# Optimization experiments

Hardware: AMD Instinct MI355X
Metric: run time of the kernel (lower is better)

The kernel has to match this reference:

```python
import jax, jax.numpy as jnp
import numpy as np

N_NODES = 100_000
N_EDGES = 800_000
NODE_DIM = 192
CONF_DIM = 64
HID = 256  # graphsage_in == graphsage_hidden
ALPHA = 0.2  # LeakyReLU negative slope


def _lrelu(x):
    return jnp.where(x >= 0, x, ALPHA * x)


def _sage_max(x, src, dst, wl, bl, wr):
    # PyG SAGEConv, aggr='max': out = lin_l(max_{j in N(i)} x_j) + lin_r(x_i)
    msgs = x[src]                                   # [E, HID] gather
    agg = jax.ops.segment_max(msgs, dst, num_segments=N_NODES)  # [N, HID]
    agg = jnp.where(jnp.isneginf(agg), 0.0, agg)    # isolated nodes -> 0
    return agg @ wl + bl + x @ wr


def _mlp2(x, w0, b0, w1, b1):
    # Linear -> LeakyReLU(0.2) -> Linear (activation only between layers)
    return _lrelu(x @ w0 + b0) @ w1 + b1


def setup_inputs() -> dict:
    key = jax.random.key(0)
    ks = jax.random.split(key, 16)
    s = 0.05
    inp = {
        "node_features": jax.random.normal(ks[0], (N_NODES, NODE_DIM), jnp.float32),
        "config_features": jax.random.normal(ks[1], (N_NODES, CONF_DIM), jnp.float32),
        "edges": jax.random.randint(ks[2], (2, N_EDGES), 0, N_NODES, jnp.int32),
        "prenet_w0": jax.random.normal(ks[3], (HID, NODE_DIM), jnp.float32) * s,
        "prenet_b0": jnp.zeros((NODE_DIM,), jnp.float32),
        "prenet_w1": jax.random.normal(ks[4], (NODE_DIM, NODE_DIM), jnp.float32) * s,
        "prenet_b1": jnp.zeros((NODE_DIM,), jnp.float32),
    }
    for l, k0 in ((0, 5), (1, 10)):
        inp[f"sage{l}_wl"] = jax.random.normal(ks[k0], (HID, HID), jnp.float32) * s
        inp[f"sage{l}_bl"] = jnp.zeros((HID,), jnp.float32)
        inp[f"sage{l}_wr"] = jax.random.normal(ks[k0 + 1], (HID, HID), jnp.float32) * s
        inp[f"mlp{l}_w0"] = jax.random.normal(ks[k0 + 2], (HID, NODE_DIM), jnp.float32) * s
        inp[f"mlp{l}_b0"] = jnp.zeros((NODE_DIM,), jnp.float32)
        inp[f"mlp{l}_w1"] = jax.random.normal(ks[k0 + 3], (NODE_DIM, NODE_DIM), jnp.float32) * s
        inp[f"mlp{l}_b1"] = jnp.zeros((NODE_DIM,), jnp.float32)
    return inp


def reference(node_features, config_features, edges,
              prenet_w0, prenet_b0, prenet_w1, prenet_b1,
              sage0_wl, sage0_bl, sage0_wr, mlp0_w0, mlp0_b0, mlp0_w1, mlp0_b1,
              sage1_wl, sage1_bl, sage1_wr, mlp1_w0, mlp1_b0, mlp1_w1, mlp1_b1):
    src, dst = edges[0], edges[1]
    x = jnp.concatenate([config_features, node_features], axis=1)  # [N, 256]
    x = _lrelu(_mlp2(x, prenet_w0, prenet_b0, prenet_w1, prenet_b1))  # [N, 192]
    layers = [
        (sage0_wl, sage0_bl, sage0_wr, mlp0_w0, mlp0_b0, mlp0_w1, mlp0_b1),
        (sage1_wl, sage1_bl, sage1_wr, mlp1_w0, mlp1_b0, mlp1_w1, mlp1_b1),
    ]
    for swl, sbl, swr, mw0, mb0, mw1, mb1 in layers:
        y = jnp.concatenate([config_features, x], axis=1)          # [N, 256]
        y = _sage_max(y, src, dst, swl, sbl, swr)                  # [N, 256]
        y = _lrelu(_mlp2(y, mw0, mb0, mw1, mb1))                   # [N, 192]
        x = x + y
    return x
```

## Files before the change

kernel.cpp:

```cpp
#include <hip/hip_runtime.h>
#include <stdint.h>

#define N_NODES 100000
#define N_EDGES 800000

typedef unsigned short u16;
typedef __attribute__((ext_vector_type(8))) short bf16x8;
typedef __attribute__((ext_vector_type(8))) unsigned short ushort8;
typedef __attribute__((ext_vector_type(4))) float f32x4;
typedef __attribute__((ext_vector_type(4))) int i32x4;
typedef __attribute__((ext_vector_type(4))) unsigned int u32x4;

struct alignas(8) U16x4 { u16 x, y, z, w; };

__device__ __forceinline__ u16 f2b(float f) {
    union { float f; unsigned u; } x; x.f = f;
    unsigned r = (x.u + 0x7FFFu + ((x.u >> 16) & 1u)) >> 16;
    return (u16)r;
}
__device__ __forceinline__ float b2f(u16 h) {
    union { unsigned u; float f; } x; x.u = ((unsigned)h) << 16;
    return x.f;
}
__device__ __forceinline__ u16 keyb(u16 h) {
    u16 m = (u16)((short)h >> 15);
    return (u16)(h ^ (0x8000u | (m & 0x7FFFu)));
}
__device__ __forceinline__ u16 unkey(u16 k) {
    u16 m = (u16)((short)k >> 15);
    return (u16)(k ^ (0x8000u | (~m & 0x7FFFu)));
}
__device__ __forceinline__ unsigned pkmax(unsigned a, unsigned b) {
    unsigned d;
    asm("v_pk_max_u16 %0, %1, %2" : "=v"(d) : "v"(a), "v"(b));
    return d;
}
__device__ __forceinline__ u32x4 pkmax4(u32x4 a, u32x4 b) {
    u32x4 r;
    r.x = pkmax(a.x, b.x); r.y = pkmax(a.y, b.y);
    r.z = pkmax(a.z, b.z); r.w = pkmax(a.w, b.w);
    return r;
}

__device__ __forceinline__ void gload_lds16(const void* g, void* l) {
    __builtin_amdgcn_global_load_lds(
        (const __attribute__((address_space(1))) char*)(uintptr_t)g,
        (__attribute__((address_space(3))) char*)(uintptr_t)l,
        16, 0, 0);
}

__device__ __forceinline__ int simgG(int row, int col) { return row * 136 + col; }
__device__ __forceinline__ int simgF(int row, int col) { return row * 200 + col; }


__global__ void k_prep(const float* __restrict__ conf, const float* __restrict__ node,
                       u16* __restrict__ conf16, u16* __restrict__ node16,
                       u16* __restrict__ keyed, int* __restrict__ deg) {
    const int c4 = N_NODES * 64 / 4;
    const int n4 = N_NODES * 192 / 4;
    int i = blockIdx.x * blockDim.x + threadIdx.x;
    if (i < c4) {
        float4 v = ((const float4*)conf)[i];
        U16x4 o; o.x = f2b(v.x); o.y = f2b(v.y); o.z = f2b(v.z); o.w = f2b(v.w);
        ((U16x4*)conf16)[i] = o;
        U16x4 ko; ko.x = keyb(o.x); ko.y = keyb(o.y); ko.z = keyb(o.z); ko.w = keyb(o.w);
        int n = i >> 4;
        ((U16x4*)keyed)[n * 64 + (i & 15)] = ko;
    } else if (i < c4 + n4) {
        float4 v = ((const float4*)node)[i - c4];
        U16x4 o; o.x = f2b(v.x); o.y = f2b(v.y); o.z = f2b(v.z); o.w = f2b(v.w);
        ((U16x4*)node16)[i - c4] = o;
    } else if (i < c4 + n4 + N_NODES / 4) {
        i32x4 z = {0, 0, 0, 0};
        ((i32x4*)deg)[i - c4 - n4] = z;
    }
}


struct PackSeg { const float* a; const float* b; u16* dst; int K0, K1, Ncol, beg, end; };
struct PackArgs { PackSeg s[8]; };

__global__ void k_pack(PackArgs p, int total) {
    int idx = blockIdx.x * blockDim.x + threadIdx.x;
    if (idx >= total) return;
    #pragma unroll
    for (int si = 0; si < 8; ++si) {
        if (idx >= p.s[si].beg && idx < p.s[si].end) {
            int li = idx - p.s[si].beg;
            int Ncol = p.s[si].Ncol, K0 = p.s[si].K0;
            int kq = li & 7;
            int t = li >> 3;
            int c15 = t & 15; t >>= 4;
            int k8 = t & 3;  t >>= 2;
            int nb = Ncol >> 4;
            int cb = t % nb;
            int ks = t / nb;
            int col = cb * 16 + c15;
            int k = ks * 32 + k8 * 8 + kq;
            float v = (k < K0) ? p.s[si].a[(size_t)k * Ncol + col]
                               : p.s[si].b[(size_t)(k - K0) * Ncol + col];
            p.s[si].dst[li] = f2b(v);
        }
    }
}


__global__ void k_count(const int* __restrict__ dst, int* __restrict__ deg) {
    int e = blockIdx.x * blockDim.x + threadIdx.x;
    if (e < N_EDGES) atomicAdd(&deg[dst[e]], 1);
}

__global__ void k_scan1(const int* __restrict__ deg, int* __restrict__ excl,
                        int* __restrict__ bsum, int n) {
    __shared__ int sh[512];
    int t = threadIdx.x;
    int base = blockIdx.x * 2048 + t * 4;
    int v0 = (base + 0 < n) ? deg[base + 0] : 0;
    int v1 = (base + 1 < n) ? deg[base + 1] : 0;
    int v2 = (base + 2 < n) ? deg[base + 2] : 0;
    int v3 = (base + 3 < n) ? deg[base + 3] : 0;
    int tot = v0 + v1 + v2 + v3;
    sh[t] = tot;
    __syncthreads();
    for (int off = 1; off < 512; off <<= 1) {
        int x = (t >= off) ? sh[t - off] : 0;
        __syncthreads();
        sh[t] += x;
        __syncthreads();
    }
    int run = sh[t] - tot;
    if (base + 0 < n) excl[base + 0] = run; run += v0;
    if (base + 1 < n) excl[base + 1] = run; run += v1;
    if (base + 2 < n) excl[base + 2] = run; run += v2;
    if (base + 3 < n) excl[base + 3] = run;
    if (t == 511) bsum[blockIdx.x] = sh[t];
}

__global__ void k_scan2(int* __restrict__ bsum, int nb) {
    __shared__ int sh[64];
    int t = threadIdx.x;
    int v = (t < nb) ? bsum[t] : 0;
    sh[t] = v;
    __syncthreads();
    for (int off = 1; off < 64; off <<= 1) {
        int x = (t >= off) ? sh[t - off] : 0;
        __syncthreads();
        sh[t] += x;
        __syncthreads();
    }
    if (t < nb) bsum[t] = sh[t] - v;
}

__global__ void k_scan3(int* __restrict__ excl, const int* __restrict__ bsum,
                        int* __restrict__ cursor, int n) {
    int i = blockIdx.x * blockDim.x + threadIdx.x;
    if (i < n) {
        int v = excl[i] + bsum[i >> 11];
        excl[i] = v;
        cursor[i] = v;
    }
}

__global__ void k_scatter(const int* __restrict__ src, const int* __restrict__ dst,
                          int* __restrict__ cursor, int* __restrict__ esrc) {
    int e = blockIdx.x * blockDim.x + threadIdx.x;
    if (e < N_EDGES) {
        int p = atomicAdd(&cursor[dst[e]], 1);
        esrc[p] = src[e];
    }
}


template<int CHUNKS>
__global__ __launch_bounds__(256) void k_agg(
    const u16* __restrict__ keyed,
    const int* __restrict__ indptr, const int* __restrict__ deg,
    const int* __restrict__ iend, const int* __restrict__ esrc,
    u16* __restrict__ agg, u16* __restrict__ aggC) {
    __shared__ int se[512];
    __shared__ int sinfo[2];
    const int b4 = blockIdx.x * 4;
    if (threadIdx.x == 0) {
        sinfo[0] = indptr[b4];
        sinfo[1] = iend[b4 + 3];
    }
    __syncthreads();
    const int sbase = sinfo[0];
    const int slen = sinfo[1] - sbase;
    const bool useLds = slen <= 512;
    if (useLds) {
        for (int i = threadIdx.x; i < slen; i += 256) se[i] = esrc[sbase + i];
    }
    __syncthreads();

    const int node = b4 + (threadIdx.x >> 6);
    const int lane = threadIdx.x & 63;
    constexpr int ACTIVE = (CHUNKS == 32) ? 64 : 48;
    const int e_sub = (CHUNKS == 32) ? (lane >> 5) : (lane >= 24 ? 1 : 0);
    int ch = lane - e_sub * CHUNKS;
    if (ch < 0 || ch >= CHUNKS) ch = 0;
    const int start = indptr[node];
    const int d = deg[node];
    const u16* bp = keyed + ((CHUNKS == 32) ? 0 : 64) + ch * 8;

    u32x4 m = {0u, 0u, 0u, 0u};

    if (lane < ACTIVE && d > 0) {
        const int rounds = (d + 15) >> 4;
        const int lbase = start - sbase;
        const int dm1 = d - 1;
        for (int rr = 0; rr < rounds; ++rr) {
            const int b0 = rr * 16 + e_sub;
            int s[8];
            if (useLds) {
                #pragma unroll
                for (int t = 0; t < 8; ++t) s[t] = se[lbase + min(b0 + 2 * t, dm1)];
            } else {
                #pragma unroll
                for (int t = 0; t < 8; ++t) s[t] = esrc[start + min(b0 + 2 * t, dm1)];
            }
            u32x4 v0 = *(const u32x4*)(bp + (size_t)s[0] * 256);
            u32x4 v1 = *(const u32x4*)(bp + (size_t)s[1] * 256);
            u32x4 v2 = *(const u32x4*)(bp + (size_t)s[2] * 256);
            u32x4 v3 = *(const u32x4*)(bp + (size_t)s[3] * 256);
            u32x4 v4 = *(const u32x4*)(bp + (size_t)s[4] * 256);
            u32x4 v5 = *(const u32x4*)(bp + (size_t)s[5] * 256);
            u32x4 v6 = *(const u32x4*)(bp + (size_t)s[6] * 256);
            u32x4 v7 = *(const u32x4*)(bp + (size_t)s[7] * 256);
            u32x4 a = pkmax4(pkmax4(v0, v1), pkmax4(v2, v3));
            u32x4 b = pkmax4(pkmax4(v4, v5), pkmax4(v6, v7));
            m = pkmax4(m, pkmax4(a, b));
        }
    }

    if (CHUNKS == 32) {
        m.x = pkmax(m.x, __shfl_xor(m.x, 32, 64));
        m.y = pkmax(m.y, __shfl_xor(m.y, 32, 64));
        m.z = pkmax(m.z, __shfl_xor(m.z, 32, 64));
        m.w = pkmax(m.w, __shfl_xor(m.w, 32, 64));
    } else {
        m.x = pkmax(m.x, __shfl(m.x, lane + 24, 64));
        m.y = pkmax(m.y, __shfl(m.y, lane + 24, 64));
        m.z = pkmax(m.z, __shfl(m.z, lane + 24, 64));
        m.w = pkmax(m.w, __shfl(m.w, lane + 24, 64));
    }

    unsigned wv[4] = {m.x, m.y, m.z, m.w};
    ushort8 o;
    #pragma unroll
    for (int j = 0; j < 4; ++j) {
        u16 klo = (u16)(wv[j] & 0xFFFFu), khi = (u16)(wv[j] >> 16);
        o[2 * j]     = (d > 0) ? unkey(klo) : (u16)0;
        o[2 * j + 1] = (d > 0) ? unkey(khi) : (u16)0;
    }

    if (CHUNKS == 32) {
        if (lane < 32) {
            *(ushort8*)(agg + (size_t)node * 256 + lane * 8) = o;
            if (lane < 8)
                *(ushort8*)(aggC + (size_t)node * 64 + lane * 8) = o;
        }
    } else {
        if (lane < 24) {
            *(ushort8*)(agg + (size_t)node * 256 + 64 + lane * 8) = o;
        } else if (lane >= 48 && lane < 56) {
            const int c2 = lane - 48;
            ushort8 v = *(const ushort8*)(aggC + (size_t)node * 64 + c2 * 8);
            *(ushort8*)(agg + (size_t)node * 256 + c2 * 8) = v;
        }
    }
}


template<int BN>
__global__ __launch_bounds__(512) void k_gemm(
    const u16* __restrict__ A0, int K0,
    const u16* __restrict__ A1, int K1,
    const u16* __restrict__ A2, int K2,
    const u16* __restrict__ Bt,
    const float* __restrict__ bias,
    u16* __restrict__ outb,
    int nrows)
{
    constexpr int FN = BN / 64;
    constexpr int ASZ = 128 * 32;
    __shared__ u16 lds[2][ASZ + BN * 32] __attribute__((aligned(16)));

    const int tid = threadIdx.x;
    const int wave = tid >> 6;
    const int lane = tid & 63;
    const int wr = wave >> 2;
    const int wc = wave & 3;
    const int rowbase = blockIdx.x * 128;
    const int nk = (K0 + K1 + K2) >> 5;

    const int arow = ((tid >> 6) << 4) | (tid & 15);
    int grow = rowbase + arow; if (grow >= nrows) grow = nrows - 1;
    const int ak8 = (tid >> 4) & 3;
    const u16* segp[3] = {A0, A1, A2};
    const int segK[3] = {K0, K1, K2};
    int seg = 0;
    const u16* gA = segp[0] + (size_t)grow * segK[0] + ak8 * 8;
    int segleft = segK[0] >> 5;
    const u16* gB0 = Bt + (size_t)tid * 8;
    const u16* gB1 = Bt + (size_t)(512 + tid) * 8;
    const int wb = wave * 512;

    auto adv = [&]() {
        gA += 32;
        if (--segleft == 0) {
            while (seg < 2) {
                ++seg;
                if (segK[seg] > 0) {
                    gA = segp[seg] + (size_t)grow * segK[seg] + ak8 * 8;
                    segleft = segK[seg] >> 5;
                    break;
                }
            }
        }
        gB0 += BN * 32;
        gB1 += BN * 32;
    };
    auto stage = [&](int buf) {
        gload_lds16(gA, &lds[buf][wb]);
        gload_lds16(gB0, &lds[buf][ASZ + wb]);
        if constexpr (BN == 256) {
            gload_lds16(gB1, &lds[buf][ASZ + 4096 + wb]);
        } else {
            if (tid < 256) gload_lds16(gB1, &lds[buf][ASZ + 4096 + wb]);
        }
    };

    f32x4 zero = {0.f, 0.f, 0.f, 0.f};
    f32x4 acc[4][FN];
    #pragma unroll
    for (int fm = 0; fm < 4; ++fm)
        #pragma unroll
        for (int fn = 0; fn < FN; ++fn)
            acc[fm][fn] = zero;

    stage(0); adv();
    __syncthreads();

    const int l15 = lane & 15, l4 = lane >> 4;

    for (int ks = 0; ks < nk; ++ks) {
        const int cur = ks & 1;
        if (ks + 1 < nk) { stage(cur ^ 1); adv(); }
        const u16* la = &lds[cur][0];
        const u16* lb = &lds[cur][ASZ];
        bf16x8 a[4], b[FN];
        #pragma unroll
        for (int fm = 0; fm < 4; ++fm)
            a[fm] = *(const bf16x8*)(la + (wr * 4 + fm) * 512 + lane * 8);
        #pragma unroll
        for (int fn = 0; fn < FN; ++fn)
            b[fn] = *(const bf16x8*)(lb + (wc * FN + fn) * 512 + lane * 8);
        #pragma unroll
        for (int fm = 0; fm < 4; ++fm)
            #pragma unroll
            for (int fn = 0; fn < FN; ++fn)
                acc[fm][fn] = __builtin_amdgcn_mfma_f32_16x16x32_bf16(a[fm], b[fn], acc[fm][fn], 0, 0, 0);
        __syncthreads();
    }

    u16* sbuf = &lds[0][0];
    #pragma unroll
    for (int chunk = 0; chunk < 2; ++chunk) {
        if ((wc >> 1) == chunk) {
            const int cbase = (wc & 1) * 64;
            #pragma unroll
            for (int fn = 0; fn < FN; ++fn) {
                const int cp = cbase + fn * 16 + l15;
                const float bs = bias[chunk * 128 + cp];
                #pragma unroll
                for (int fm = 0; fm < 4; ++fm) {
                    const int rbase = wr * 64 + fm * 16 + l4 * 4;
                    #pragma unroll
                    for (int r = 0; r < 4; ++r)
                        sbuf[simgG(rbase + r, cp)] = f2b(acc[fm][fn][r] + bs);
                }
            }
        }
        __syncthreads();
        #pragma unroll
        for (int j = 0; j < 4; ++j) {
            const int chk = j * 512 + tid;
            const int row = chk >> 4;
            const int cp = (chk & 15) * 8;
            const int gr = rowbase + row;
            if (gr < nrows) {
                ushort8 hv = *(const ushort8*)&sbuf[simgG(row, cp)];
                *(ushort8*)(outb + (size_t)gr * 256 + chunk * 128 + cp) = hv;
            }
        }
        __syncthreads();
    }
}


template<int EPI>
__global__ __launch_bounds__(512) void k_fused(
    const u16* __restrict__ A0, int K0,
    const u16* __restrict__ A1, int K1,
    const u16* __restrict__ B1t, const float* __restrict__ bias1,
    const u16* __restrict__ B2t, const float* __restrict__ bias2,
    float* __restrict__ outf, u16* __restrict__ outb,
    const u16* __restrict__ resid16, u16* __restrict__ keyed,
    int nrows)
{
    __shared__ u16 lds[25592] __attribute__((aligned(16)));

    const int tid = threadIdx.x;
    const int wave = tid >> 6;
    const int lane = tid & 63;
    const int wr = wave >> 2;
    const int wc = wave & 3;
    const int l15 = lane & 15, l4 = lane >> 4;
    const int rowbase = blockIdx.x * 128;
    const int nk1 = (K0 + K1) >> 5;

    const int arow = ((tid >> 6) << 4) | (tid & 15);
    int grow = rowbase + arow; if (grow >= nrows) grow = nrows - 1;
    const int ak8 = (tid >> 4) & 3;
    const u16* gA = A0 + (size_t)grow * K0 + ak8 * 8;
    int segleft = K0 >> 5;
    const u16* gB0 = B1t + (size_t)tid * 8;
    const u16* gB1 = B1t + (size_t)(512 + tid) * 8;
    const int wb = wave * 512;

    auto adv = [&]() {
        gA += 32;
        if (--segleft == 0 && K1 > 0) {
            gA = A1 + (size_t)grow * K1 + ak8 * 8;
            segleft = K1 >> 5;
        }
        gB0 += 6144;
        gB1 += 6144;
    };
    auto stage = [&](int buf) {
        gload_lds16(gA, &lds[buf * 4096 + wb]);
        gload_lds16(gB0, &lds[8192 + buf * 6144 + wb]);
        if (tid < 256) gload_lds16(gB1, &lds[8192 + buf * 6144 + 4096 + wb]);
    };

    f32x4 zero = {0.f, 0.f, 0.f, 0.f};
    f32x4 acc[4][3];
    #pragma unroll
    for (int fm = 0; fm < 4; ++fm)
        #pragma unroll
        for (int fn = 0; fn < 3; ++fn)
            acc[fm][fn] = zero;

    stage(0); adv();
    __syncthreads();

    for (int ks = 0; ks < nk1; ++ks) {
        const int cur = ks & 1;
        if (ks + 1 < nk1) { stage(cur ^ 1); adv(); }
        const u16* la = &lds[cur * 4096];
        const u16* lb = &lds[8192 + cur * 6144];
        bf16x8 a[4], b[3];
        #pragma unroll
        for (int fm = 0; fm < 4; ++fm)
            a[fm] = *(const bf16x8*)(la + (wr * 4 + fm) * 512 + lane * 8);
        #pragma unroll
        for (int fn = 0; fn < 3; ++fn)
            b[fn] = *(const bf16x8*)(lb + (wc * 3 + fn) * 512 + lane * 8);
        #pragma unroll
        for (int fm = 0; fm < 4; ++fm)
            #pragma unroll
            for (int fn = 0; fn < 3; ++fn)
                acc[fm][fn] = __builtin_amdgcn_mfma_f32_16x16x32_bf16(a[fm], b[fn], acc[fm][fn], 0, 0, 0);
        __syncthreads();
    }

    {
        const int c0 = wc * 48;
        #pragma unroll
        for (int fn = 0; fn < 3; ++fn) {
            const int c = c0 + fn * 16 + l15;
            const float bs = bias1[c];
            const int coff = (c >> 5) * 4096 + ((c >> 3) & 3) * 128 + (c & 7);
            #pragma unroll
            for (int fm = 0; fm < 4; ++fm) {
                const int rb = wr * 4 + fm;
                #pragma unroll
                for (int rr = 0; rr < 4; ++rr) {
                    const int r16 = l4 * 4 + rr;
                    float v = acc[fm][fn][rr] + bs;
                    v = (v >= 0.f) ? v : 0.2f * v;
                    lds[coff + rb * 512 + r16 * 8] = f2b(v);
                }
            }
        }
    }
    __syncthreads();

    bf16x8 breg[18];
    #pragma unroll
    for (int ks = 0; ks < 6; ++ks)
        #pragma unroll
        for (int fn = 0; fn < 3; ++fn)
            breg[ks * 3 + fn] = *(const bf16x8*)(B2t + (size_t)(ks * 12 + wc * 3 + fn) * 512 + lane * 8);

    f32x4 acc2[4][3];
    #pragma unroll
    for (int fm = 0; fm < 4; ++fm)
        #pragma unroll
        for (int fn = 0; fn < 3; ++fn)
            acc2[fm][fn] = zero;

    #pragma unroll
    for (int ks = 0; ks < 6; ++ks) {
        bf16x8 a2[4];
        #pragma unroll
        for (int fm = 0; fm < 4; ++fm)
            a2[fm] = *(const bf16x8*)(&lds[ks * 4096 + (wr * 4 + fm) * 512 + lane * 8]);
        #pragma unroll
        for (int fm = 0; fm < 4; ++fm)
            #pragma unroll
            for (int fn = 0; fn < 3; ++fn)
                acc2[fm][fn] = __builtin_amdgcn_mfma_f32_16x16x32_bf16(a2[fm], breg[ks * 3 + fn], acc2[fm][fn], 0, 0, 0);
    }
    __syncthreads();

    {
        const int c0 = wc * 48;
        #pragma unroll
        for (int fn = 0; fn < 3; ++fn) {
            const int c = c0 + fn * 16 + l15;
            const float bs = bias2[c];
            #pragma unroll
            for (int fm = 0; fm < 4; ++fm) {
                const int rbase = wr * 64 + fm * 16 + l4 * 4;
                #pragma unroll
                for (int r = 0; r < 4; ++r) {
                    float v = acc2[fm][fn][r] + bs;
                    v = (v >= 0.f) ? v : 0.2f * v;
                    lds[simgF(rbase + r, c)] = f2b(v);
                }
            }
        }
    }
    __syncthreads();

    #pragma unroll
    for (int j = 0; j < 6; ++j) {
        const int chk = j * 512 + tid;
        const int row = chk / 24;
        const int c = (chk - row * 24) * 8;
        const int gr = rowbase + row;
        if (gr < nrows) {
            ushort8 hv = *(const ushort8*)&lds[simgF(row, c)];
            if (EPI == 4) {
                ushort8 rv = *(const ushort8*)(resid16 + (size_t)gr * 192 + c);
                f32x4 o0, o1;
                #pragma unroll
                for (int k = 0; k < 4; ++k) {
                    o0[k] = b2f(hv[k]) + b2f(rv[k]);
                    o1[k] = b2f(hv[k + 4]) + b2f(rv[k + 4]);
                }
                *(f32x4*)(outf + (size_t)gr * 192 + c) = o0;
                *(f32x4*)(outf + (size_t)gr * 192 + c + 4) = o1;
            } else if (EPI == 5) {
                *(ushort8*)(outb + (size_t)gr * 192 + c) = hv;
                ushort8 kv;
                #pragma unroll
                for (int k = 0; k < 8; ++k) kv[k] = keyb(hv[k]);
                *(ushort8*)(keyed + (size_t)gr * 256 + 64 + c) = kv;
            } else {
                ushort8 rv = *(const ushort8*)(resid16 + (size_t)gr * 192 + c);
                ushort8 nb, kv;
                #pragma unroll
                for (int k = 0; k < 8; ++k) {
                    u16 hb = f2b(b2f(hv[k]) + b2f(rv[k]));
                    nb[k] = hb;
                    kv[k] = keyb(hb);
                }
                *(ushort8*)(outb + (size_t)gr * 192 + c) = nb;
                *(ushort8*)(keyed + (size_t)gr * 256 + 64 + c) = kv;
            }
        }
    }
}


extern "C" void kernel_launch(void* const* d_in, const int* in_sizes, int n_in,
                              void* d_out, int out_size, void* d_ws, size_t ws_size,
                              hipStream_t stream)
{
    (void)in_sizes; (void)n_in; (void)out_size; (void)ws_size;
    const float* node = (const float*)d_in[0];
    const float* conf = (const float*)d_in[1];
    const int* edges  = (const int*)d_in[2];
    const float* pw0  = (const float*)d_in[3];
    const float* pb0  = (const float*)d_in[4];
    const float* pw1  = (const float*)d_in[5];
    const float* pb1  = (const float*)d_in[6];
    const float* W[14];
    for (int i = 0; i < 14; ++i) W[i] = (const float*)d_in[7 + i];
    float* out = (float*)d_out;
    const int* e_src = edges;
    const int* e_dst = edges + N_EDGES;

    u16* keyed = (u16*)d_out;

    char* w = (char*)d_ws;
    auto alloc = [&](size_t b) { char* p = w; w += (b + 255) & ~(size_t)255; return p; };
    u16* conf16 = (u16*)alloc((size_t)N_NODES * 64 * 2);
    u16* node16 = (u16*)alloc((size_t)N_NODES * 192 * 2);
    u16* x16    = (u16*)alloc((size_t)N_NODES * 192 * 2);
    u16* agg16  = (u16*)alloc((size_t)N_NODES * 256 * 2);
    u16* aggC   = (u16*)alloc((size_t)N_NODES * 64 * 2);
    int* deg    = (int*)alloc((size_t)N_NODES * 4);
    int* indptr = (int*)alloc((size_t)N_NODES * 4);
    int* cursor = (int*)alloc((size_t)N_NODES * 4);
    int* esrc   = (int*)alloc((size_t)N_EDGES * 4);
    int* bsum   = (int*)alloc(4096);
    u16* pw0t   = (u16*)alloc((size_t)192 * 256 * 2);
    u16* pw1t   = (u16*)alloc((size_t)192 * 192 * 2);
    u16 *sB[2], *mw0t[2], *mw1t[2];
    for (int l = 0; l < 2; ++l) {
        sB[l]   = (u16*)alloc((size_t)256 * 512 * 2);
        mw0t[l] = (u16*)alloc((size_t)192 * 256 * 2);
        mw1t[l] = (u16*)alloc((size_t)192 * 192 * 2);
    }

    {
        const int tot = N_NODES * 64 / 4 + N_NODES * 192 / 4 + N_NODES / 4;
        k_prep<<<(tot + 255) / 256, 256, 0, stream>>>(conf, node, conf16, node16, keyed, deg);
    }
    {
        PackArgs pa;
        int off = 0;
        auto seg = [&](int i, const float* a, int K0, const float* b, int K1, int Ncol, u16* dst) {
            int sz = Ncol * (K0 + K1);
            pa.s[i] = {a, b, dst, K0, K1, Ncol, off, off + sz};
            off += sz;
        };
        seg(0, pw0, 256, nullptr, 0, 192, pw0t);
        seg(1, pw1, 192, nullptr, 0, 192, pw1t);
        seg(2, W[0], 256, W[2], 256, 256, sB[0]);
        seg(3, W[3], 256, nullptr, 0, 192, mw0t[0]);
        seg(4, W[5], 192, nullptr, 0, 192, mw1t[0]);
        seg(5, W[7], 256, W[9], 256, 256, sB[1]);
        seg(6, W[10], 256, nullptr, 0, 192, mw0t[1]);
        seg(7, W[12], 192, nullptr, 0, 192, mw1t[1]);
        k_pack<<<(off + 255) / 256, 256, 0, stream>>>(pa, off);
    }
    k_count<<<(N_EDGES + 255) / 256, 256, 0, stream>>>(e_dst, deg);
    int nb = (N_NODES + 2047) / 2048;
    k_scan1<<<nb, 512, 0, stream>>>(deg, indptr, bsum, N_NODES);
    k_scan2<<<1, 64, 0, stream>>>(bsum, nb);
    k_scan3<<<(N_NODES + 255) / 256, 256, 0, stream>>>(indptr, bsum, cursor, N_NODES);
    k_scatter<<<(N_EDGES + 255) / 256, 256, 0, stream>>>(e_src, e_dst, cursor, esrc);

    const int gblk = (N_NODES + 127) / 128;
    k_fused<5><<<gblk, 512, 0, stream>>>(conf16, 64, node16, 192,
                                         pw0t, pb0, pw1t, pb1,
                                         nullptr, x16, nullptr, keyed, N_NODES);
    for (int l = 0; l < 2; ++l) {
        if (l == 0)
            k_agg<32><<<N_NODES / 4, 256, 0, stream>>>(keyed, indptr, deg, cursor, esrc, agg16, aggC);
        else
            k_agg<24><<<N_NODES / 4, 256, 0, stream>>>(keyed, indptr, deg, cursor, esrc, agg16, aggC);
        k_gemm<256><<<gblk, 512, 0, stream>>>(agg16, 256, conf16, 64, x16, 192,
                                              sB[l], W[7*l+1], agg16, N_NODES);
        if (l == 0)
            k_fused<6><<<gblk, 512, 0, stream>>>(agg16, 256, nullptr, 0,
                                                 mw0t[0], W[4], mw1t[0], W[6],
                                                 nullptr, x16, x16, keyed, N_NODES);
        else
            k_fused<4><<<gblk, 512, 0, stream>>>(agg16, 256, nullptr, 0,
                                                 mw0t[1], W[11], mw1t[1], W[13],
                                                 out, nullptr, x16, nullptr, N_NODES);
    }
}
```

Before: 444.8 us.

## Merge weight packing into prep, persistent agg grid, read conf agg via strided GEMM segments

Folds the weight-packing kernel into the input-prep kernel to save a launch. Makes the aggregation kernel grid-stride over node quads with a fixed 2048-block grid instead of one block per quad. Generalises the GEMM A-operand to four strided segments so layer 1 reads the config aggregate from aggC directly, which removes the per-node copy of aggC into agg16. The persistent loop adds an extra barrier per quad and may reduce latency hiding in the gather.

```diff
diff --git a/kernel.cpp b/kernel.cpp
--- a/kernel.cpp
+++ b/kernel.cpp
@@ -53,9 +53,14 @@
 __device__ __forceinline__ int simgF(int row, int col) { return row * 200 + col; }
 
 
+struct PackSeg { const float* a; const float* b; u16* dst; int K0, K1, Ncol, beg, end; };
+struct PackArgs { PackSeg s[8]; };
+
+
 __global__ void k_prep(const float* __restrict__ conf, const float* __restrict__ node,
                        u16* __restrict__ conf16, u16* __restrict__ node16,
-                       u16* __restrict__ keyed, int* __restrict__ deg) {
+                       u16* __restrict__ keyed, int* __restrict__ deg,
+                       PackArgs p, int packTotal) {
     const int c4 = N_NODES * 64 / 4;
     const int n4 = N_NODES * 192 / 4;
     int i = blockIdx.x * blockDim.x + threadIdx.x;
@@ -73,33 +78,28 @@
     } else if (i < c4 + n4 + N_NODES / 4) {
         i32x4 z = {0, 0, 0, 0};
         ((i32x4*)deg)[i - c4 - n4] = z;
-    }
-}
-
-
-struct PackSeg { const float* a; const float* b; u16* dst; int K0, K1, Ncol, beg, end; };
-struct PackArgs { PackSeg s[8]; };
-
-__global__ void k_pack(PackArgs p, int total) {
-    int idx = blockIdx.x * blockDim.x + threadIdx.x;
-    if (idx >= total) return;
-    #pragma unroll
-    for (int si = 0; si < 8; ++si) {
-        if (idx >= p.s[si].beg && idx < p.s[si].end) {
-            int li = idx - p.s[si].beg;
-            int Ncol = p.s[si].Ncol, K0 = p.s[si].K0;
-            int kq = li & 7;
-            int t = li >> 3;
-            int c15 = t & 15; t >>= 4;
-            int k8 = t & 3;  t >>= 2;
-            int nb = Ncol >> 4;
-            int cb = t % nb;
-            int ks = t / nb;
-            int col = cb * 16 + c15;
-            int k = ks * 32 + k8 * 8 + kq;
-            float v = (k < K0) ? p.s[si].a[(size_t)k * Ncol + col]
-                               : p.s[si].b[(size_t)(k - K0) * Ncol + col];
-            p.s[si].dst[li] = f2b(v);
+    } else {
+        int idx = i - (c4 + n4 + N_NODES / 4);
+        if (idx < packTotal) {
+            #pragma unroll
+            for (int si = 0; si < 8; ++si) {
+                if (idx >= p.s[si].beg && idx < p.s[si].end) {
+                    int li = idx - p.s[si].beg;
+                    int Ncol = p.s[si].Ncol, K0 = p.s[si].K0;
+                    int kq = li & 7;
+                    int t = li >> 3;
+                    int c15 = t & 15; t >>= 4;
+                    int k8 = t & 3;  t >>= 2;
+                    int nb = Ncol >> 4;
+                    int cb = t % nb;
+                    int ks = t / nb;
+                    int col = cb * 16 + c15;
+                    int k = ks * 32 + k8 * 8 + kq;
+                    float v = (k < K0) ? p.s[si].a[(size_t)k * Ncol + col]
+                                       : p.s[si].b[(size_t)(k - K0) * Ncol + col];
+                    p.s[si].dst[li] = f2b(v);
+                }
+            }
         }
     }
 }
@@ -176,107 +176,106 @@
     const u16* __restrict__ keyed,
     const int* __restrict__ indptr, const int* __restrict__ deg,
     const int* __restrict__ iend, const int* __restrict__ esrc,
-    u16* __restrict__ agg, u16* __restrict__ aggC) {
+    u16* __restrict__ agg, u16* __restrict__ aggC, int nquads) {
     __shared__ int se[512];
     __shared__ int sinfo[2];
-    const int b4 = blockIdx.x * 4;
-    if (threadIdx.x == 0) {
-        sinfo[0] = indptr[b4];
-        sinfo[1] = iend[b4 + 3];
-    }
-    __syncthreads();
-    const int sbase = sinfo[0];
-    const int slen = sinfo[1] - sbase;
-    const bool useLds = slen <= 512;
-    if (useLds) {
-        for (int i = threadIdx.x; i < slen; i += 256) se[i] = esrc[sbase + i];
-    }
-    __syncthreads();
-
-    const int node = b4 + (threadIdx.x >> 6);
     const int lane = threadIdx.x & 63;
     constexpr int ACTIVE = (CHUNKS == 32) ? 64 : 48;
     const int e_sub = (CHUNKS == 32) ? (lane >> 5) : (lane >= 24 ? 1 : 0);
     int ch = lane - e_sub * CHUNKS;
     if (ch < 0 || ch >= CHUNKS) ch = 0;
-    const int start = indptr[node];
-    const int d = deg[node];
     const u16* bp = keyed + ((CHUNKS == 32) ? 0 : 64) + ch * 8;
 
-    u32x4 m = {0u, 0u, 0u, 0u};
-
-    if (lane < ACTIVE && d > 0) {
-        const int rounds = (d + 15) >> 4;
-        const int lbase = start - sbase;
-        const int dm1 = d - 1;
-        for (int rr = 0; rr < rounds; ++rr) {
-            const int b0 = rr * 16 + e_sub;
-            int s[8];
-            if (useLds) {
-                #pragma unroll
-                for (int t = 0; t < 8; ++t) s[t] = se[lbase + min(b0 + 2 * t, dm1)];
-            } else {
-                #pragma unroll
-                for (int t = 0; t < 8; ++t) s[t] = esrc[start + min(b0 + 2 * t, dm1)];
-            }
-            u32x4 v0 = *(const u32x4*)(bp + (size_t)s[0] * 256);
-            u32x4 v1 = *(const u32x4*)(bp + (size_t)s[1] * 256);
-            u32x4 v2 = *(const u32x4*)(bp + (size_t)s[2] * 256);
-            u32x4 v3 = *(const u32x4*)(bp + (size_t)s[3] * 256);
-            u32x4 v4 = *(const u32x4*)(bp + (size_t)s[4] * 256);
-            u32x4 v5 = *(const u32x4*)(bp + (size_t)s[5] * 256);
-            u32x4 v6 = *(const u32x4*)(bp + (size_t)s[6] * 256);
-            u32x4 v7 = *(const u32x4*)(bp + (size_t)s[7] * 256);
-            u32x4 a = pkmax4(pkmax4(v0, v1), pkmax4(v2, v3));
-            u32x4 b = pkmax4(pkmax4(v4, v5), pkmax4(v6, v7));
-            m = pkmax4(m, pkmax4(a, b));
-        }
-    }
-
-    if (CHUNKS == 32) {
-        m.x = pkmax(m.x, __shfl_xor(m.x, 32, 64));
-        m.y = pkmax(m.y, __shfl_xor(m.y, 32, 64));
-        m.z = pkmax(m.z, __shfl_xor(m.z, 32, 64));
-        m.w = pkmax(m.w, __shfl_xor(m.w, 32, 64));
-    } else {
-        m.x = pkmax(m.x, __shfl(m.x, lane + 24, 64));
-        m.y = pkmax(m.y, __shfl(m.y, lane + 24, 64));
-        m.z = pkmax(m.z, __shfl(m.z, lane + 24, 64));
-        m.w = pkmax(m.w, __shfl(m.w, lane + 24, 64));
-    }
-
-    unsigned wv[4] = {m.x, m.y, m.z, m.w};
-    ushort8 o;
-    #pragma unroll
-    for (int j = 0; j < 4; ++j) {
-        u16 klo = (u16)(wv[j] & 0xFFFFu), khi = (u16)(wv[j] >> 16);
-        o[2 * j]     = (d > 0) ? unkey(klo) : (u16)0;
-        o[2 * j + 1] = (d > 0) ? unkey(khi) : (u16)0;
-    }
-
-    if (CHUNKS == 32) {
-        if (lane < 32) {
-            *(ushort8*)(agg + (size_t)node * 256 + lane * 8) = o;
-            if (lane < 8)
-                *(ushort8*)(aggC + (size_t)node * 64 + lane * 8) = o;
-        }
-    } else {
-        if (lane < 24) {
-            *(ushort8*)(agg + (size_t)node * 256 + 64 + lane * 8) = o;
-        } else if (lane >= 48 && lane < 56) {
-            const int c2 = lane - 48;
-            ushort8 v = *(const ushort8*)(aggC + (size_t)node * 64 + c2 * 8);
-            *(ushort8*)(agg + (size_t)node * 256 + c2 * 8) = v;
-        }
-    }
-}
-
+    for (int q = blockIdx.x; q < nquads; q += gridDim.x) {
+        const int b4 = q * 4;
+        if (threadIdx.x == 0) {
+            sinfo[0] = indptr[b4];
+            sinfo[1] = iend[b4 + 3];
+        }
+        __syncthreads();
+        const int sbase = sinfo[0];
+        const int slen = sinfo[1] - sbase;
+        const bool useLds = slen <= 512;
+        if (useLds) {
+            for (int i = threadIdx.x; i < slen; i += 256) se[i] = esrc[sbase + i];
+        }
+        __syncthreads();
+
+        const int node = b4 + (threadIdx.x >> 6);
+        const int start = indptr[node];
+        const int d = deg[node];
+
+        u32x4 m = {0u, 0u, 0u, 0u};
+
+        if (lane < ACTIVE && d > 0) {
+            const int rounds = (d + 15) >> 4;
+            const int lbase = start - sbase;
+            const int dm1 = d - 1;
+            for (int rr = 0; rr < rounds; ++rr) {
+                const int b0 = rr * 16 + e_sub;
+                int s[8];
+                if (useLds) {
+                    #pragma unroll
+                    for (int t = 0; t < 8; ++t) s[t] = se[lbase + min(b0 + 2 * t, dm1)];
+                } else {
+                    #pragma unroll
+                    for (int t = 0; t < 8; ++t) s[t] = esrc[start + min(b0 + 2 * t, dm1)];
+                }
+                u32x4 v0 = *(const u32x4*)(bp + (size_t)s[0] * 256);
+                u32x4 v1 = *(const u32x4*)(bp + (size_t)s[1] * 256);
+                u32x4 v2 = *(const u32x4*)(bp + (size_t)s[2] * 256);
+                u32x4 v3 = *(const u32x4*)(bp + (size_t)s[3] * 256);
+                u32x4 v4 = *(const u32x4*)(bp + (size_t)s[4] * 256);
+                u32x4 v5 = *(const u32x4*)(bp + (size_t)s[5] * 256);
+                u32x4 v6 = *(const u32x4*)(bp + (size_t)s[6] * 256);
+                u32x4 v7 = *(const u32x4*)(bp + (size_t)s[7] * 256);
+                u32x4 a = pkmax4(pkmax4(v0, v1), pkmax4(v2, v3));
+                u32x4 b = pkmax4(pkmax4(v4, v5), pkmax4(v6, v7));
+                m = pkmax4(m, pkmax4(a, b));
+            }
+        }
+
+        if (CHUNKS == 32) {
+            m.x = pkmax(m.x, __shfl_xor(m.x, 32, 64));
+            m.y = pkmax(m.y, __shfl_xor(m.y, 32, 64));
+            m.z = pkmax(m.z, __shfl_xor(m.z, 32, 64));
+            m.w = pkmax(m.w, __shfl_xor(m.w, 32, 64));
+        } else {
+            m.x = pkmax(m.x, __shfl(m.x, lane + 24, 64));
+            m.y = pkmax(m.y, __shfl(m.y, lane + 24, 64));
+            m.z = pkmax(m.z, __shfl(m.z, lane + 24, 64));
+            m.w = pkmax(m.w, __shfl(m.w, lane + 24, 64));
+        }
+
+        unsigned wv[4] = {m.x, m.y, m.z, m.w};
+        ushort8 o;
+        #pragma unroll
+        for (int j = 0; j < 4; ++j) {
+            u16 klo = (u16)(wv[j] & 0xFFFFu), khi = (u16)(wv[j] >> 16);
+            o[2 * j]     = (d > 0) ? unkey(klo) : (u16)0;
+            o[2 * j + 1] = (d > 0) ? unkey(khi) : (u16)0;
+        }
+
+        if (CHUNKS == 32) {
+            if (lane < 32) {
+                *(ushort8*)(agg + (size_t)node * 256 + lane * 8) = o;
+                if (lane < 8)
+                    *(ushort8*)(aggC + (size_t)node * 64 + lane * 8) = o;
+            }
+        } else {
+            if (lane < 24)
+                *(ushort8*)(agg + (size_t)node * 256 + 64 + lane * 8) = o;
+        }
+        __syncthreads();
+    }
+}
+
+
+struct SegA { const u16* p; int K; int stride; };
 
 template<int BN>
 __global__ __launch_bounds__(512) void k_gemm(
-    const u16* __restrict__ A0, int K0,
-    const u16* __restrict__ A1, int K1,
-    const u16* __restrict__ A2, int K2,
+    SegA s0, SegA s1, SegA s2, SegA s3,
     const u16* __restrict__ Bt,
     const float* __restrict__ bias,
     u16* __restrict__ outb,
@@ -292,15 +291,16 @@
     const int wr = wave >> 2;
     const int wc = wave & 3;
     const int rowbase = blockIdx.x * 128;
-    const int nk = (K0 + K1 + K2) >> 5;
+    const u16* segp[4] = {s0.p, s1.p, s2.p, s3.p};
+    const int segK[4]  = {s0.K, s1.K, s2.K, s3.K};
+    const int segS[4]  = {s0.stride, s1.stride, s2.stride, s3.stride};
+    const int nk = (segK[0] + segK[1] + segK[2] + segK[3]) >> 5;
 
     const int arow = ((tid >> 6) << 4) | (tid & 15);
     int grow = rowbase + arow; if (grow >= nrows) grow = nrows - 1;
     const int ak8 = (tid >> 4) & 3;
-    const u16* segp[3] = {A0, A1, A2};
-    const int segK[3] = {K0, K1, K2};
     int seg = 0;
-    const u16* gA = segp[0] + (size_t)grow * segK[0] + ak8 * 8;
+    const u16* gA = segp[0] + (size_t)grow * segS[0] + ak8 * 8;
     int segleft = segK[0] >> 5;
     const u16* gB0 = Bt + (size_t)tid * 8;
     const u16* gB1 = Bt + (size_t)(512 + tid) * 8;
@@ -309,10 +309,10 @@
     auto adv = [&]() {
         gA += 32;
         if (--segleft == 0) {
-            while (seg < 2) {
+            while (seg < 3) {
                 ++seg;
                 if (segK[seg] > 0) {
-                    gA = segp[seg] + (size_t)grow * segK[seg] + ak8 * 8;
+                    gA = segp[seg] + (size_t)grow * segS[seg] + ak8 * 8;
                     segleft = segK[seg] >> 5;
                     break;
                 }
@@ -628,10 +628,6 @@
     }
 
     {
-        const int tot = N_NODES * 64 / 4 + N_NODES * 192 / 4 + N_NODES / 4;
-        k_prep<<<(tot + 255) / 256, 256, 0, stream>>>(conf, node, conf16, node16, keyed, deg);
-    }
-    {
         PackArgs pa;
         int off = 0;
         auto seg = [&](int i, const float* a, int K0, const float* b, int K1, int Ncol, u16* dst) {
@@ -647,7 +643,9 @@
         seg(5, W[7], 256, W[9], 256, 256, sB[1]);
         seg(6, W[10], 256, nullptr, 0, 192, mw0t[1]);
         seg(7, W[12], 192, nullptr, 0, 192, mw1t[1]);
-        k_pack<<<(off + 255) / 256, 256, 0, stream>>>(pa, off);
+        const int tot = N_NODES * 64 / 4 + N_NODES * 192 / 4 + N_NODES / 4 + off;
+        k_prep<<<(tot + 255) / 256, 256, 0, stream>>>(conf, node, conf16, node16,
+                                                      keyed, deg, pa, off);
     }
     k_count<<<(N_EDGES + 255) / 256, 256, 0, stream>>>(e_dst, deg);
     int nb = (N_NODES + 2047) / 2048;
@@ -657,16 +655,26 @@
     k_scatter<<<(N_EDGES + 255) / 256, 256, 0, stream>>>(e_src, e_dst, cursor, esrc);
 
     const int gblk = (N_NODES + 127) / 128;
+    const int nquads = N_NODES / 4;
     k_fused<5><<<gblk, 512, 0, stream>>>(conf16, 64, node16, 192,
                                          pw0t, pb0, pw1t, pb1,
                                          nullptr, x16, nullptr, keyed, N_NODES);
     for (int l = 0; l < 2; ++l) {
-        if (l == 0)
-            k_agg<32><<<N_NODES / 4, 256, 0, stream>>>(keyed, indptr, deg, cursor, esrc, agg16, aggC);
-        else
-            k_agg<24><<<N_NODES / 4, 256, 0, stream>>>(keyed, indptr, deg, cursor, esrc, agg16, aggC);
-        k_gemm<256><<<gblk, 512, 0, stream>>>(agg16, 256, conf16, 64, x16, 192,
-                                              sB[l], W[7*l+1], agg16, N_NODES);
+        if (l == 0) {
+            k_agg<32><<<2048, 256, 0, stream>>>(keyed, indptr, deg, cursor, esrc,
+                                                agg16, aggC, nquads);
+            k_gemm<256><<<gblk, 512, 0, stream>>>(
+                SegA{agg16, 256, 256}, SegA{conf16, 64, 64},
+                SegA{x16, 192, 192}, SegA{nullptr, 0, 0},
+                sB[0], W[1], agg16, N_NODES);
+        } else {
+            k_agg<24><<<2048, 256, 0, stream>>>(keyed, indptr, deg, cursor, esrc,
+                                                agg16, aggC, nquads);
+            k_gemm<256><<<gblk, 512, 0, stream>>>(
+                SegA{aggC, 64, 64}, SegA{agg16 + 64, 192, 256},
+                SegA{conf16, 64, 64}, SegA{x16, 192, 192},
+                sB[1], W[8], agg16, N_NODES);
+        }
         if (l == 0)
             k_fused<6><<<gblk, 512, 0, stream>>>(agg16, 256, nullptr, 0,
                                                  mw0t[0], W[4], mw1t[0], W[6],
```

Measured after the change: 446.0 us. No clear change (+0.3%).
